# Kernel tuning notes

Measured on AMD Instinct MI355X. Metric: run time of the kernel, lower is better.

The kernel has to match this reference:

```python
import jax, jax.numpy as jnp
import numpy as np
from jax import lax

D_MODEL = 1024
D_STATE = 16
D_CONV = 4
EXPAND = 2
D_INNER = EXPAND * D_MODEL           # 2048 (mamba inner)
DT_RANK = (D_MODEL + 15) // 16       # 64
D_FF = 4 * D_MODEL                   # 4096 (SwiGLU hidden)
EPS = 1e-5
B, L = 2, 2048


def setup_inputs() -> dict:
    key = jax.random.key(0)
    ks = jax.random.split(key, 16)
    s = 0.02
    inp = {
        'x': jax.random.normal(ks[0], (B, L, D_MODEL), jnp.float32),
        'norm1_w': jnp.ones((D_MODEL,), jnp.float32),
        'norm2_w': jnp.ones((D_MODEL,), jnp.float32),
        # Mamba params (torch Linear convention: y = x @ W.T)
        'in_proj_w': s * jax.random.normal(ks[1], (2 * D_INNER, D_MODEL), jnp.float32),
        'conv_w': s * jax.random.normal(ks[2], (D_INNER, 1, D_CONV), jnp.float32),
        'conv_b': jnp.zeros((D_INNER,), jnp.float32),
        'x_proj_w': s * jax.random.normal(ks[3], (DT_RANK + 2 * D_STATE, D_INNER), jnp.float32),
        'dt_proj_w': s * jax.random.normal(ks[4], (D_INNER, DT_RANK), jnp.float32),
        'dt_proj_b': jax.random.uniform(ks[5], (D_INNER,), jnp.float32, -4.0, -2.0),
        'A_log': jnp.log(jnp.broadcast_to(jnp.arange(1, D_STATE + 1, dtype=jnp.float32), (D_INNER, D_STATE))),
        'D': jnp.ones((D_INNER,), jnp.float32),
        'out_proj_w': s * jax.random.normal(ks[6], (D_MODEL, D_INNER), jnp.float32),
        # SwiGLU MLP
        'w1': s * jax.random.normal(ks[7], (D_FF, D_MODEL), jnp.float32),
        'w2': s * jax.random.normal(ks[8], (D_FF, D_MODEL), jnp.float32),
        'w3': s * jax.random.normal(ks[9], (D_MODEL, D_FF), jnp.float32),
    }
    return inp


def _rmsnorm(x, w, eps=EPS):
    return x * lax.rsqrt(jnp.mean(x * x, axis=-1, keepdims=True) + eps) * w


def _mamba(x, in_proj_w, conv_w, conv_b, x_proj_w, dt_proj_w, dt_proj_b, A_log, Dp, out_proj_w):
    # x: (B, L, d_model)
    xz = x @ in_proj_w.T                       # (B, L, 2*d_inner)
    u, z = jnp.split(xz, 2, axis=-1)           # each (B, L, d_inner)
    # causal depthwise conv1d over time
    u_nch = u.transpose(0, 2, 1)               # (B, d_inner, L)
    u_conv = lax.conv_general_dilated(
        u_nch, conv_w, window_strides=(1,), padding=[(D_CONV - 1, 0)],
        dimension_numbers=('NCH', 'OIH', 'NCH'), feature_group_count=D_INNER)
    u_conv = u_conv + conv_b[None, :, None]
    u_act = jax.nn.silu(u_conv.transpose(0, 2, 1))   # (B, L, d_inner)
    # input-dependent dt, B, C
    proj = u_act @ x_proj_w.T                  # (B, L, dt_rank + 2*d_state)
    dt_r, Bm, Cm = jnp.split(proj, [DT_RANK, DT_RANK + D_STATE], axis=-1)
    dt = jax.nn.softplus(dt_r @ dt_proj_w.T + dt_proj_b)   # (B, L, d_inner)
    A = -jnp.exp(A_log)                        # (d_inner, d_state)
    dA = jnp.exp(jnp.einsum('bld,dn->bldn', dt, A))
    dBu = jnp.einsum('bld,bln,bld->bldn', dt, Bm, u_act)
    def step(h, inputs):
        dA_t, dBu_t = inputs                   # (B, d_inner, d_state)
        h = dA_t * h + dBu_t
        return h, h
    h0 = jnp.zeros((x.shape[0], D_INNER, D_STATE), x.dtype)
    _, hs = lax.scan(step, h0, (dA.transpose(1, 0, 2, 3), dBu.transpose(1, 0, 2, 3)))
    y = jnp.einsum('lbdn,bln->bld', hs, Cm) + u_act * Dp   # (B, L, d_inner)
    y = y * jax.nn.silu(z)
    return y @ out_proj_w.T                    # (B, L, d_model)


def reference(x, norm1_w, norm2_w, in_proj_w, conv_w, conv_b, x_proj_w,
              dt_proj_w, dt_proj_b, A_log, D, out_proj_w, w1, w2, w3):
    # residual + RMSNorm + Mamba (dropout = eval-mode identity)
    h = x + _mamba(_rmsnorm(x, norm1_w), in_proj_w, conv_w, conv_b,
                   x_proj_w, dt_proj_w, dt_proj_b, A_log, D, out_proj_w)
    # residual + RMSNorm + SwiGLU MLP
    xn = _rmsnorm(h, norm2_w)
    mlp = (jax.nn.silu(xn @ w1.T) * (xn @ w2.T)) @ w3.T
    return h + mlp
```

## Files before the change

### kernel.cpp

```cpp
#include <hip/hip_runtime.h>
#include <hip/hip_bf16.h>

#define TOKS 4096
#define DM   1024
#define DI   2048
#define DST  16
#define DTR  64
#define DFF  4096
#define PROJ_LD 128

#define NC    32
#define CHUNK 64

typedef __bf16 bf16x8 __attribute__((ext_vector_type(8)));
typedef float  f32x4  __attribute__((ext_vector_type(4)));

__device__ __forceinline__ __bf16 f2bf(float f) {
  union { float f; unsigned u; } v; v.f = f;
  unsigned r = v.u + 0x7fffu + ((v.u >> 16) & 1u);
  union { unsigned short s; __bf16 b; } o; o.s = (unsigned short)(r >> 16);
  return o.b;
}
__device__ __forceinline__ float siluf(float x) { return x / (1.f + __expf(-x)); }
__device__ __forceinline__ float softplusf(float x) { return x > 20.f ? x : log1pf(__expf(x)); }

__device__ __forceinline__ void gl2lds16(const void* g, void* l) {
  __builtin_amdgcn_global_load_lds((const __attribute__((address_space(1))) void*)g,
                                   (__attribute__((address_space(3))) void*)l, 16, 0, 0);
}

struct CvtArgs {
  const float* src[5];
  __bf16*      dst[5];
  int nblk[6];
};

__global__ __launch_bounds__(256) void cvt_bf16_kernel(CvtArgs a) {
  int blk = blockIdx.x;
  int seg = 0;
#pragma unroll
  for (int s = 1; s < 5; s++) if (blk >= a.nblk[s]) seg = s;
  size_t base = (size_t)(blk - a.nblk[seg]) * 2048 + threadIdx.x * 8;
  const float* src = a.src[seg] + base;
  __bf16*      dst = a.dst[seg] + base;
  float4 v0 = *(const float4*)src;
  float4 v1 = *(const float4*)(src + 4);
  union { __bf16 b[8]; uint4 u; } t;
  t.b[0]=f2bf(v0.x); t.b[1]=f2bf(v0.y); t.b[2]=f2bf(v0.z); t.b[3]=f2bf(v0.w);
  t.b[4]=f2bf(v1.x); t.b[5]=f2bf(v1.y); t.b[6]=f2bf(v1.z); t.b[7]=f2bf(v1.w);
  *(uint4*)dst = t.u;
}

__global__ __launch_bounds__(256) void cvt_w12_kernel(const float* __restrict__ w1,
                                                      const float* __restrict__ w2,
                                                      __bf16* __restrict__ dst) {
  int blk = blockIdx.x;
  int isw2 = blk >> 11;
  int b = blk & 2047;
  int r = b * 2 + (threadIdx.x >> 7);
  int col = (threadIdx.x & 127) * 8;
  const float* src = (isw2 ? w2 : w1) + (size_t)r * DM + col;
  int dr = (r >> 4) * 32 + (r & 15) + isw2 * 16;
  float4 v0 = *(const float4*)src;
  float4 v1 = *(const float4*)(src + 4);
  union { __bf16 b[8]; uint4 u; } t;
  t.b[0]=f2bf(v0.x); t.b[1]=f2bf(v0.y); t.b[2]=f2bf(v0.z); t.b[3]=f2bf(v0.w);
  t.b[4]=f2bf(v1.x); t.b[5]=f2bf(v1.y); t.b[6]=f2bf(v1.z); t.b[7]=f2bf(v1.w);
  *(uint4*)&dst[(size_t)dr * DM + col] = t.u;
}

__global__ __launch_bounds__(256) void rmsnorm_kernel(const float* __restrict__ x,
                                                      const float* __restrict__ w,
                                                      __bf16* __restrict__ out) {
  int row = blockIdx.x;
  const float* xr = x + (size_t)row * DM;
  float4 v = ((const float4*)xr)[threadIdx.x];
  float ss = v.x*v.x + v.y*v.y + v.z*v.z + v.w*v.w;
#pragma unroll
  for (int o = 32; o > 0; o >>= 1) ss += __shfl_xor(ss, o);
  __shared__ float sred[4];
  if ((threadIdx.x & 63) == 0) sred[threadIdx.x >> 6] = ss;
  __syncthreads();
  float tot = sred[0] + sred[1] + sred[2] + sred[3];
  float scale = rsqrtf(tot * (1.f / DM) + 1e-5f);
  float4 wv = ((const float4*)w)[threadIdx.x];
  union { __bf16 b[4]; ushort4 u; } o;
  o.b[0] = f2bf(v.x * scale * wv.x);
  o.b[1] = f2bf(v.y * scale * wv.y);
  o.b[2] = f2bf(v.z * scale * wv.z);
  o.b[3] = f2bf(v.w * scale * wv.w);
  *(ushort4*)&out[(size_t)row * DM + threadIdx.x * 4] = o.u;
}

template<int BM, int EPI, int SWAP, int KK, int Z, int LDA, int LDB, int LDC>
__global__ __launch_bounds__(256, BM == 128 ? 1 : 2) void gemm2(
    const void* __restrict__ Ap, const __bf16* __restrict__ Bp,
    void* __restrict__ Cp, const void* __restrict__ auxp)
{
  constexpr int FM = BM / 32;
  constexpr int AI = BM / 64;
  constexpr int kPer = KK / Z;
  __shared__ __bf16 sA[2][BM * 32];
  __shared__ __bf16 sB[2][128 * 32];
  const int tid  = threadIdx.x;
  const int wave = tid >> 6, lane = tid & 63;
  const int bm = SWAP ? blockIdx.x : blockIdx.y;
  const int bn = SWAP ? blockIdx.y : blockIdx.x;
  const int m0 = bm * BM, n0 = bn * 128;
  const int wr = wave >> 1, wc = wave & 1;
  const int frow = lane & 15, fq = lane >> 4;

  f32x4 acc[FM][4] = {};

  const int kBeg = (Z > 1) ? blockIdx.z * kPer : 0;
  const int kEnd = kBeg + kPer;

  const int lrow = lane >> 2;
  const int lcol = (lane & 3) * 8;

  auto stage = [&](int kt, int buf) {
#pragma unroll
    for (int q = 0; q < AI; q++) {
      int idx = wave * AI + q;
      gl2lds16((const __bf16*)Ap + (size_t)(m0 + idx * 16 + lrow) * LDA + kt + lcol,
               &sA[buf][idx * 512]);
    }
#pragma unroll
    for (int q = 0; q < 2; q++) {
      int idx = wave * 2 + q;
      gl2lds16(Bp + (size_t)(n0 + idx * 16 + lrow) * LDB + kt + lcol,
               &sB[buf][idx * 512]);
    }
  };

  stage(kBeg, 0);
  int cur = 0;
  for (int kt = kBeg; kt < kEnd; kt += 32) {
    __syncthreads();

    bf16x8 afr[FM], bfr[4];
#pragma unroll
    for (int i = 0; i < FM; i++)
      afr[i] = *(const bf16x8*)&sA[cur][(wr * (BM/2) + i * 16 + frow) * 32 + fq * 8];
#pragma unroll
    for (int j = 0; j < 4; j++)
      bfr[j] = *(const bf16x8*)&sB[cur][(wc * 64 + j * 16 + frow) * 32 + fq * 8];

    if (kt + 32 < kEnd) stage(kt + 32, cur ^ 1);

#pragma unroll
    for (int i = 0; i < FM; i++)
#pragma unroll
      for (int j = 0; j < 4; j++)
        acc[i][j] = __builtin_amdgcn_mfma_f32_16x16x32_bf16(afr[i], bfr[j], acc[i][j], 0, 0, 0);
    cur ^= 1;
  }

  const float* auxf = (const float*)auxp;
#pragma unroll
  for (int i = 0; i < FM; i++) {
    int gr = m0 + wr * (BM/2) + i * 16 + fq * 4;
#pragma unroll
    for (int j = 0; j < 4; j++) {
      int gc = n0 + wc * 64 + j * 16 + frow;
#pragma unroll
      for (int r = 0; r < 4; r++) {
        float v = acc[i][j][r];
        if (EPI == 6) {
          if (j & 1) {
            int col = (n0 >> 1) + 32 * wc + 16 * (j >> 1) + frow;
            size_t off = (size_t)(gr + r) * LDC + col;
            float g = acc[i][j-1][r];
            ((__bf16*)Cp)[off] = f2bf(siluf(g) * v);
          }
        } else {
          size_t off = (size_t)(gr + r) * LDC + gc;
          if (EPI == 1) ((__bf16*)Cp)[off] = f2bf(v);
          else if (EPI == 2) ((__bf16*)Cp)[off] = f2bf(softplusf(v + auxf[gc]));
          else if (EPI == 3) ((float*)Cp)[off] = v + auxf[off];
          else if (EPI == 7)
            ((float*)Cp)[(size_t)blockIdx.z * (TOKS * PROJ_LD) + off] = v;
        }
      }
    }
  }
}

template<int EPI, int KK, int LDA, int LDB, int LDC>
__global__ __launch_bounds__(512, 2) void gemm8(
    const __bf16* __restrict__ Ap, const __bf16* __restrict__ Bp,
    void* __restrict__ Cp)
{
  constexpr int NT = KK / 64;
  static_assert(NT % 2 == 0 && NT >= 4, "KK must be a multiple of 128");
  __shared__ alignas(16) char S[131072];

  const int tid  = threadIdx.x;
  const int wid  = tid >> 6, lane = tid & 63;
  const int wr   = wid >> 2, wc = wid & 3;
  const int m0   = blockIdx.y * 256, n0 = blockIdx.x * 256;
  const int frow = lane & 15, fq = lane >> 4;
  const int cbyt = (fq * 16) ^ (((lane >> 3) & 1) << 5);
  const int srow = lane >> 2;
  const int skin = ((lane & 3) * 8) ^ (((lane >> 5) & 1) << 4);

  const unsigned sbase = (unsigned)(size_t)(__attribute__((address_space(3))) char*)S;
  const unsigned abase = sbase + (unsigned)((wr * 64 + frow) * 64 + cbyt);
  const unsigned bbase = sbase + 32768u + (unsigned)((wc * 32 + frow) * 64 + cbyt);

  f32x4 acc[2][2][4][2] = {};
  bf16x8 fA[4][2], fB0[2][2], fB1[2][2];

#define G8_SB() __builtin_amdgcn_sched_barrier(0)
#define G8_BAR() do { G8_SB(); __builtin_amdgcn_s_barrier(); G8_SB(); } while (0)
#define G8_LGKM0() do { asm volatile("s_waitcnt lgkmcnt(0)"); G8_SB(); } while (0)
#define G8_THROT() asm volatile("s_waitcnt lgkmcnt(8)")
#define G8_WAIT6() asm volatile("s_waitcnt vmcnt(6)")
#define G8_WAIT0() asm volatile("s_waitcnt vmcnt(0)")
#define G8_DSR(dst, addr, OFF)                                                 \
    asm volatile("ds_read_b128 %0, %1 offset:" OFF : "=v"(dst) : "v"(addr))

#define G8_STAGE(buf, ab, h, tile) do {                                        \
    if ((tile) < NT) {                                                         \
      const __bf16* gb = (ab) ? Bp : Ap;                                       \
      const int ld = (ab) ? LDB : LDA;                                         \
      const int r0 = ((ab) ? n0 : m0) + (h) * 128;                             \
      _Pragma("unroll")                                                        \
      for (int q = 0; q < 2; q++) {                                            \
        int p = wid * 2 + q, kk = p >> 3, r16 = p & 7;                         \
        const __bf16* src = gb + (size_t)(r0 + r16 * 16 + srow) * ld           \
                            + (tile) * 64 + kk * 32 + skin;                    \
        char* dst = S + (((buf) * 4 + (ab) * 2 + kk) << 14)                    \
                    + ((h) * 128 + r16 * 16) * 64;                             \
        gl2lds16(src, dst);                                                    \
      }                                                                        \
    }                                                                          \
  } while (0)

#define G8_READ_A(buf, mh) do {                                                \
    unsigned a_ = abase + (buf) * 65536u + (mh) * 8192u;                       \
    f32x4 t0,t1,t2,t3,t4,t5,t6,t7;                                             \
    G8_DSR(t0, a_, "0");     G8_DSR(t1, a_, "1024");                           \
    G8_DSR(t2, a_, "2048");  G8_DSR(t3, a_, "3072");                           \
    G8_DSR(t4, a_, "16384"); G8_DSR(t5, a_, "17408");                          \
    G8_DSR(t6, a_, "18432"); G8_DSR(t7, a_, "19456");                          \
    fA[0][0]=__builtin_bit_cast(bf16x8,t0); fA[1][0]=__builtin_bit_cast(bf16x8,t1); \
    fA[2][0]=__builtin_bit_cast(bf16x8,t2); fA[3][0]=__builtin_bit_cast(bf16x8,t3); \
    fA[0][1]=__builtin_bit_cast(bf16x8,t4); fA[1][1]=__builtin_bit_cast(bf16x8,t5); \
    fA[2][1]=__builtin_bit_cast(bf16x8,t6); fA[3][1]=__builtin_bit_cast(bf16x8,t7); \
  } while (0)

#define G8_READ_B(buf, nh, FB) do {                                            \
    unsigned b_ = bbase + (buf) * 65536u + (nh) * 8192u;                       \
    f32x4 t0,t1,t2,t3;                                                         \
    G8_DSR(t0, b_, "0");     G8_DSR(t1, b_, "1024");                           \
    G8_DSR(t2, b_, "16384"); G8_DSR(t3, b_, "17408");                          \
    FB[0][0]=__builtin_bit_cast(bf16x8,t0); FB[1][0]=__builtin_bit_cast(bf16x8,t1); \
    FB[0][1]=__builtin_bit_cast(bf16x8,t2); FB[1][1]=__builtin_bit_cast(bf16x8,t3); \
  } while (0)

#define G8_MFMA(mh, nh, FB) do {                                               \
    __builtin_amdgcn_s_setprio(1);                                             \
    _Pragma("unroll")                                                          \
    for (int kk = 0; kk < 2; kk++)                                             \
      _Pragma("unroll")                                                        \
      for (int fi = 0; fi < 4; fi++)                                           \
        _Pragma("unroll")                                                      \
        for (int fj = 0; fj < 2; fj++)                                         \
          acc[mh][nh][fi][fj] = __builtin_amdgcn_mfma_f32_16x16x32_bf16(       \
              fA[fi][kk], FB[fj][kk], acc[mh][nh][fi][fj], 0, 0, 0);           \
    __builtin_amdgcn_s_setprio(0);                                             \
    G8_SB();                                                                   \
  } while (0)

  G8_STAGE(0, 0, 0, 0); G8_STAGE(0, 1, 1, 0); G8_STAGE(0, 0, 1, 0); G8_STAGE(0, 1, 0, 0);
  G8_STAGE(1, 0, 0, 1); G8_STAGE(1, 1, 1, 1); G8_STAGE(1, 0, 1, 1);
  G8_SB();
  G8_WAIT6();
  G8_BAR();

  for (int it = 0; it < NT / 2; ++it) {
    const int t1 = 2 * it + 1, t2 = 2 * it + 2, t3 = 2 * it + 3;
    const bool last = (it == NT / 2 - 1);
    G8_READ_A(0, 0); G8_READ_B(0, 0, fB0);
    G8_STAGE(1, 1, 0, t1);
    G8_SB(); G8_THROT();
    G8_BAR();
    G8_LGKM0();
    G8_MFMA(0, 0, fB0);
    G8_BAR();
    G8_READ_B(0, 1, fB1);
    G8_STAGE(0, 0, 0, t2);
    G8_SB();
    G8_BAR();
    G8_LGKM0();
    G8_MFMA(0, 1, fB1);
    G8_BAR();
    G8_READ_A(0, 1);
    G8_STAGE(0, 1, 1, t2);
    G8_SB();
    G8_BAR();
    G8_LGKM0();
    G8_MFMA(1, 1, fB1);
    G8_BAR();
    G8_STAGE(0, 0, 1, t2);
    G8_SB();
    if (last) G8_WAIT0(); else G8_WAIT6();
    G8_BAR();
    G8_MFMA(1, 0, fB0);
    G8_BAR();
    G8_READ_A(1, 0); G8_READ_B(1, 0, fB0);
    G8_STAGE(0, 1, 0, t2);
    G8_SB(); G8_THROT();
    G8_BAR();
    G8_LGKM0();
    G8_MFMA(0, 0, fB0);
    G8_BAR();
    G8_READ_B(1, 1, fB1);
    G8_STAGE(1, 0, 0, t3);
    G8_SB();
    G8_BAR();
    G8_LGKM0();
    G8_MFMA(0, 1, fB1);
    G8_BAR();
    G8_READ_A(1, 1);
    G8_STAGE(1, 1, 1, t3);
    G8_SB();
    G8_BAR();
    G8_LGKM0();
    G8_MFMA(1, 1, fB1);
    G8_BAR();
    G8_STAGE(1, 0, 1, t3);
    G8_SB();
    if (!last) G8_WAIT6();
    G8_BAR();
    G8_MFMA(1, 0, fB0);
    G8_BAR();
  }

#undef G8_STAGE
#undef G8_READ_A
#undef G8_READ_B
#undef G8_MFMA
#undef G8_BAR
#undef G8_SB
#undef G8_LGKM0
#undef G8_THROT
#undef G8_WAIT6
#undef G8_WAIT0
#undef G8_DSR

#pragma unroll
  for (int mh = 0; mh < 2; mh++)
#pragma unroll
    for (int nh = 0; nh < 2; nh++)
#pragma unroll
      for (int fi = 0; fi < 4; fi++) {
        int gr = m0 + mh * 128 + wr * 64 + fi * 16 + fq * 4;
        if constexpr (EPI == 1) {
#pragma unroll
          for (int fj = 0; fj < 2; fj++) {
            int gc = n0 + nh * 128 + wc * 32 + fj * 16 + frow;
#pragma unroll
            for (int r = 0; r < 4; r++)
              ((__bf16*)Cp)[(size_t)(gr + r) * LDC + gc] = f2bf(acc[mh][nh][fi][fj][r]);
          }
        } else {
          int col = ((n0 + nh * 128 + wc * 32) >> 1) + frow;
#pragma unroll
          for (int r = 0; r < 4; r++) {
            float g = acc[mh][nh][fi][0][r];
            float v = acc[mh][nh][fi][1][r];
            ((__bf16*)Cp)[(size_t)(gr + r) * LDC + col] = f2bf(siluf(g) * v);
          }
        }
      }
}

__global__ __launch_bounds__(256) void xp_reduce_kernel(const float* __restrict__ part,
                                                        float* __restrict__ proj,
                                                        __bf16* __restrict__ projb) {
  int i = blockIdx.x * 256 + threadIdx.x;
  float4 s = ((const float4*)part)[i];
#pragma unroll
  for (int z = 1; z < 8; z++) {
    float4 v = ((const float4*)(part + (size_t)z * TOKS * PROJ_LD))[i];
    s.x += v.x; s.y += v.y; s.z += v.z; s.w += v.w;
  }
  ((float4*)proj)[i] = s;
  int c4 = i & 31;
  if (c4 < 16) {
    int tok = i >> 5;
    union { __bf16 b[4]; ushort4 u; } t;
    t.b[0]=f2bf(s.x); t.b[1]=f2bf(s.y); t.b[2]=f2bf(s.z); t.b[3]=f2bf(s.w);
    *(ushort4*)&projb[(size_t)tok * 64 + c4 * 4] = t.u;
  }
}

__global__ __launch_bounds__(256) void conv_silu_kernel(const __bf16* __restrict__ xz,
                                                        const float* __restrict__ cw,
                                                        const float* __restrict__ cb,
                                                        __bf16* __restrict__ uact) {
  int idx = blockIdx.x * 256 + threadIdx.x;
  int d   = idx & (DI - 1);
  int tok = idx >> 11;
  int l   = tok & 2047;
  float4 wv = *(const float4*)(cw + d * 4);
  const __bf16* up = xz + (size_t)tok * (2 * DI) + d;
  float acc = cb[d];
  if (l >= 3) acc += wv.x * (float)up[-3 * (2 * DI)];
  if (l >= 2) acc += wv.y * (float)up[-2 * (2 * DI)];
  if (l >= 1) acc += wv.z * (float)up[-1 * (2 * DI)];
  acc += wv.w * (float)up[0];
  uact[idx] = f2bf(siluf(acc));
}

__global__ __launch_bounds__(64) void scan_pass1(const __bf16* __restrict__ dt,
                                                 const __bf16* __restrict__ uact,
                                                 const float* __restrict__ proj,
                                                 const float* __restrict__ A_log,
                                                 float* __restrict__ aprod,
                                                 float* __restrict__ hend) {
  int lane = threadIdx.x;
  int d = blockIdx.x * 64 + lane;
  int c = blockIdx.y, b = blockIdx.z;
  float An[16], h[16], ap[16];
  {
    const float4* a4 = (const float4*)(A_log + (size_t)d * 16);
#pragma unroll
    for (int q = 0; q < 4; q++) {
      float4 v = a4[q];
      An[q*4+0] = -__expf(v.x); An[q*4+1] = -__expf(v.y);
      An[q*4+2] = -__expf(v.z); An[q*4+3] = -__expf(v.w);
    }
  }
#pragma unroll
  for (int n = 0; n < 16; n++) { h[n] = 0.f; ap[n] = 1.f; }

  size_t tok = (size_t)b * 2048 + (size_t)c * CHUNK;
  const __bf16* dtp = dt   + tok * DI + d;
  const __bf16* up  = uact + tok * DI + d;
  const float*  pp  = proj + tok * PROJ_LD;

  for (int t = 0; t < CHUNK; t++) {
    float dtv = (float)*dtp;
    float uv  = (float)*up;
    const float4* b4 = (const float4*)(pp + 64);
    float Bv[16];
#pragma unroll
    for (int q = 0; q < 4; q++) {
      float4 v = b4[q];
      Bv[q*4+0]=v.x; Bv[q*4+1]=v.y; Bv[q*4+2]=v.z; Bv[q*4+3]=v.w;
    }
    float du = dtv * uv;
#pragma unroll
    for (int n = 0; n < 16; n++) {
      float dA = __expf(dtv * An[n]);
      ap[n] *= dA;
      h[n] = fmaf(dA, h[n], du * Bv[n]);
    }
    dtp += DI; up += DI; pp += PROJ_LD;
  }

  size_t off = ((size_t)(b * NC + c) * DI + d) * 16;
#pragma unroll
  for (int q = 0; q < 4; q++) {
    *(float4*)(hend  + off + q*4) = make_float4(h[q*4+0],  h[q*4+1],  h[q*4+2],  h[q*4+3]);
    *(float4*)(aprod + off + q*4) = make_float4(ap[q*4+0], ap[q*4+1], ap[q*4+2], ap[q*4+3]);
  }
}

__global__ __launch_bounds__(256) void scan_pass2(const float* __restrict__ aprod,
                                                  const float* __restrict__ hend,
                                                  float* __restrict__ hstart) {
  int idx = blockIdx.x * 256 + threadIdx.x;
  int b  = idx >> 13;
  int r4 = idx & 8191;
  float4 H = make_float4(0.f, 0.f, 0.f, 0.f);
  for (int c = 0; c < NC; c++) {
    size_t off = (size_t)(b * NC + c) * (DI * 16 / 4) + r4;
    ((float4*)hstart)[off] = H;
    float4 a = ((const float4*)aprod)[off];
    float4 e = ((const float4*)hend)[off];
    H.x = fmaf(a.x, H.x, e.x);
    H.y = fmaf(a.y, H.y, e.y);
    H.z = fmaf(a.z, H.z, e.z);
    H.w = fmaf(a.w, H.w, e.w);
  }
}

__global__ __launch_bounds__(64) void scan_pass3(const __bf16* __restrict__ dt,
                                                 const __bf16* __restrict__ uact,
                                                 const float* __restrict__ proj,
                                                 const __bf16* __restrict__ xz,
                                                 const float* __restrict__ A_log,
                                                 const float* __restrict__ Dp,
                                                 const float* __restrict__ hstart,
                                                 __bf16* __restrict__ y) {
  int lane = threadIdx.x;
  int d = blockIdx.x * 64 + lane;
  int c = blockIdx.y, b = blockIdx.z;
  float An[16], h[16];
  {
    const float4* a4 = (const float4*)(A_log + (size_t)d * 16);
#pragma unroll
    for (int q = 0; q < 4; q++) {
      float4 v = a4[q];
      An[q*4+0] = -__expf(v.x); An[q*4+1] = -__expf(v.y);
      An[q*4+2] = -__expf(v.z); An[q*4+3] = -__expf(v.w);
    }
  }
  {
    size_t off = ((size_t)(b * NC + c) * DI + d) * 16;
#pragma unroll
    for (int q = 0; q < 4; q++) {
      float4 v = *(const float4*)(hstart + off + q*4);
      h[q*4+0]=v.x; h[q*4+1]=v.y; h[q*4+2]=v.z; h[q*4+3]=v.w;
    }
  }
  float Dd = Dp[d];

  size_t tok = (size_t)b * 2048 + (size_t)c * CHUNK;
  const __bf16* dtp = dt   + tok * DI + d;
  const __bf16* up  = uact + tok * DI + d;
  const float*  pp  = proj + tok * PROJ_LD;
  const __bf16* zp  = xz   + tok * (2 * DI) + DI + d;
  __bf16*       yp  = y    + tok * DI + d;

  for (int t = 0; t < CHUNK; t++) {
    float dtv = (float)*dtp;
    float uv  = (float)*up;
    float zv  = (float)*zp;
    const float4* b4 = (const float4*)(pp + 64);
    float Bv[16], Cv[16];
#pragma unroll
    for (int q = 0; q < 4; q++) {
      float4 v = b4[q];
      Bv[q*4+0]=v.x; Bv[q*4+1]=v.y; Bv[q*4+2]=v.z; Bv[q*4+3]=v.w;
      float4 w = b4[q + 4];
      Cv[q*4+0]=w.x; Cv[q*4+1]=w.y; Cv[q*4+2]=w.z; Cv[q*4+3]=w.w;
    }
    float du = dtv * uv;
    float p = 0.f;
#pragma unroll
    for (int n = 0; n < 16; n++) {
      float dA = __expf(dtv * An[n]);
      h[n] = fmaf(dA, h[n], du * Bv[n]);
      p = fmaf(h[n], Cv[n], p);
    }
    *yp = f2bf((p + Dd * uv) * siluf(zv));
    dtp += DI; up += DI; pp += PROJ_LD; zp += 2 * DI; yp += DI;
  }
}

extern "C" void kernel_launch(void* const* d_in, const int* in_sizes, int n_in,
                              void* d_out, int out_size, void* d_ws, size_t ws_size,
                              hipStream_t stream) {
  const float* x        = (const float*)d_in[0];
  const float* n1w      = (const float*)d_in[1];
  const float* n2w      = (const float*)d_in[2];
  const float* in_projw = (const float*)d_in[3];
  const float* conv_w   = (const float*)d_in[4];
  const float* conv_b   = (const float*)d_in[5];
  const float* x_projw  = (const float*)d_in[6];
  const float* dt_projw = (const float*)d_in[7];
  const float* dt_projb = (const float*)d_in[8];
  const float* A_log    = (const float*)d_in[9];
  const float* Dp       = (const float*)d_in[10];
  const float* out_projw= (const float*)d_in[11];
  const float* w1       = (const float*)d_in[12];
  const float* w2       = (const float*)d_in[13];
  const float* w3       = (const float*)d_in[14];
  float* out = (float*)d_out;

  char* ws = (char*)d_ws;
  __bf16* xz   = (__bf16*)(ws + 0);
  __bf16* uact = (__bf16*)(ws + 33554432);
  float*  proj = (float*) (ws + 50331648);
  __bf16* dt   = (__bf16*)(ws + 52428800);
  __bf16* yb   = (__bf16*)(ws + 85983232);
  float*  xpp  = (float*) (ws + 85983232);
  float*  h    = (float*) (ws + 102760448);
  __bf16* xn   = (__bf16*)(ws + 119537664);
  __bf16* hid  = xz;
  __bf16* projb = (__bf16*)(ws + 102760448);
  float* aprod  = (float*)(ws + 102760448);
  float* hend   = (float*)(ws + 111149056);
  float* hstart = (float*)(ws + 119537664);
  char* wb = ws + 127926272;
  __bf16* b_in  = (__bf16*)(wb);
  __bf16* b_xp  = (__bf16*)(wb + 8388608);
  __bf16* b_dtp = (__bf16*)(wb + 8912896);
  __bf16* b_out = (__bf16*)(wb + 9175040);
  __bf16* b_w12 = (__bf16*)(wb + 13369344);
  __bf16* b_w3  = (__bf16*)(wb + 30146560);

  hipMemsetAsync(b_xp, 0, 128 * 2048 * sizeof(__bf16), stream);

  CvtArgs ca;
  const float* srcs[5] = {in_projw, x_projw, dt_projw, out_projw, w3};
  __bf16* dsts[5]      = {b_in, b_xp, b_dtp, b_out, b_w3};
  int counts[5] = {4096*1024, 96*2048, 2048*64, 1024*2048, 1024*4096};
  int acc = 0;
  for (int i = 0; i < 5; i++) { ca.src[i] = srcs[i]; ca.dst[i] = dsts[i]; ca.nblk[i] = acc; acc += counts[i] / 2048; }
  ca.nblk[5] = acc;
  cvt_bf16_kernel<<<acc, 256, 0, stream>>>(ca);
  cvt_w12_kernel<<<4096, 256, 0, stream>>>(w1, w2, b_w12);

  dim3 blk(256);
  rmsnorm_kernel<<<TOKS, 256, 0, stream>>>(x, n1w, xn);
  gemm8<1, 1024, DM, DM, 4096><<<dim3(16, 16), 512, 0, stream>>>(xn, b_in, xz);
  conv_silu_kernel<<<(TOKS*DI)/256, 256, 0, stream>>>(xz, conv_w, conv_b, uact);
  gemm2<64,7,0, 2048,8, DI,DI,PROJ_LD><<<dim3(1,64,8), blk, 0, stream>>>(uact, b_xp, xpp, nullptr);
  xp_reduce_kernel<<<512, 256, 0, stream>>>(xpp, proj, projb);
  gemm2<128,2,0, 64,1, 64,DTR,DI><<<dim3(16,32,1), blk, 0, stream>>>(projb, b_dtp, dt, dt_projb);
  scan_pass1<<<dim3(DI/64, NC, 2), 64, 0, stream>>>(dt, uact, proj, A_log, aprod, hend);
  scan_pass2<<<64, 256, 0, stream>>>(aprod, hend, hstart);
  scan_pass3<<<dim3(DI/64, NC, 2), 64, 0, stream>>>(dt, uact, proj, xz, A_log, Dp, hstart, yb);
  gemm2<64,3,1, 2048,1, DI,DI,DM><<<dim3(64,8,1), blk, 0, stream>>>(yb, b_out, h, x);
  rmsnorm_kernel<<<TOKS, 256, 0, stream>>>(h, n2w, xn);
  gemm8<6, 1024, DM, DM, DFF><<<dim3(32, 16), 512, 0, stream>>>(xn, b_w12, hid);
  gemm2<64,3,1, 4096,1, DFF,DFF,DM><<<dim3(64,8,1), blk, 0, stream>>>(hid, b_w3, out, h);

  (void)in_sizes; (void)n_in; (void)out_size; (void)ws_size;
}
```

Baseline: 522.5 us.

## Split-K the output GEMMs, fuse reduction with residual and RMSNorm, vectorize conv

Measured after the change: 536.7 us. +2.7%, slower.

```diff
diff --git a/kernel.cpp b/kernel.cpp
--- a/kernel.cpp
+++ b/kernel.cpp
@@ -92,8 +92,49 @@
   *(ushort4*)&out[(size_t)row * DM + threadIdx.x * 4] = o.u;
 }
 
+__global__ __launch_bounds__(256) void rmsnorm_red3_kernel(const float* __restrict__ p,
+                                                           const float* __restrict__ xres,
+                                                           const float* __restrict__ w,
+                                                           float* __restrict__ hout,
+                                                           __bf16* __restrict__ out) {
+  int row = blockIdx.x;
+  size_t base = (size_t)row * DM + threadIdx.x * 4;
+  float4 a = *(const float4*)(p + base);
+  float4 b = *(const float4*)(p + (size_t)TOKS * DM + base);
+  float4 c = *(const float4*)(xres + base);
+  float4 v = make_float4(a.x + b.x + c.x, a.y + b.y + c.y,
+                         a.z + b.z + c.z, a.w + b.w + c.w);
+  *(float4*)(hout + base) = v;
+  float ss = v.x*v.x + v.y*v.y + v.z*v.z + v.w*v.w;
+#pragma unroll
+  for (int o = 32; o > 0; o >>= 1) ss += __shfl_xor(ss, o);
+  __shared__ float sred[4];
+  if ((threadIdx.x & 63) == 0) sred[threadIdx.x >> 6] = ss;
+  __syncthreads();
+  float tot = sred[0] + sred[1] + sred[2] + sred[3];
+  float scale = rsqrtf(tot * (1.f / DM) + 1e-5f);
+  float4 wv = ((const float4*)w)[threadIdx.x];
+  union { __bf16 b[4]; ushort4 u; } o;
+  o.b[0] = f2bf(v.x * scale * wv.x);
+  o.b[1] = f2bf(v.y * scale * wv.y);
+  o.b[2] = f2bf(v.z * scale * wv.z);
+  o.b[3] = f2bf(v.w * scale * wv.w);
+  *(ushort4*)&out[base] = o.u;
+}
+
+__global__ __launch_bounds__(256) void add_red2_kernel(const float* __restrict__ p,
+                                                       const float* __restrict__ aux,
+                                                       float* __restrict__ out) {
+  int i = blockIdx.x * 256 + threadIdx.x;
+  float4 a = ((const float4*)p)[i];
+  float4 b = ((const float4*)(p + (size_t)TOKS * DM))[i];
+  float4 c = ((const float4*)aux)[i];
+  ((float4*)out)[i] = make_float4(a.x + b.x + c.x, a.y + b.y + c.y,
+                                  a.z + b.z + c.z, a.w + b.w + c.w);
+}
+
 template<int BM, int EPI, int SWAP, int KK, int Z, int LDA, int LDB, int LDC>
-__global__ __launch_bounds__(256, BM == 128 ? 1 : 2) void gemm2(
+__global__ __launch_bounds__(256, BM == 128 ? 1 : 4) void gemm2(
     const void* __restrict__ Ap, const __bf16* __restrict__ Bp,
     void* __restrict__ Cp, const void* __restrict__ auxp)
 {
@@ -180,6 +221,8 @@
           else if (EPI == 3) ((float*)Cp)[off] = v + auxf[off];
           else if (EPI == 7)
             ((float*)Cp)[(size_t)blockIdx.z * (TOKS * PROJ_LD) + off] = v;
+          else if (EPI == 8)
+            ((float*)Cp)[(size_t)blockIdx.z * ((size_t)TOKS * LDC) + off] = v;
         }
       }
     }
@@ -402,17 +445,30 @@
                                                         const float* __restrict__ cb,
                                                         __bf16* __restrict__ uact) {
   int idx = blockIdx.x * 256 + threadIdx.x;
-  int d   = idx & (DI - 1);
-  int tok = idx >> 11;
+  int d8  = (idx & 255) * 8;
+  int tok = idx >> 8;
   int l   = tok & 2047;
-  float4 wv = *(const float4*)(cw + d * 4);
-  const __bf16* up = xz + (size_t)tok * (2 * DI) + d;
-  float acc = cb[d];
-  if (l >= 3) acc += wv.x * (float)up[-3 * (2 * DI)];
-  if (l >= 2) acc += wv.y * (float)up[-2 * (2 * DI)];
-  if (l >= 1) acc += wv.z * (float)up[-1 * (2 * DI)];
-  acc += wv.w * (float)up[0];
-  uact[idx] = f2bf(siluf(acc));
+  const __bf16* up = xz + (size_t)tok * (2 * DI) + d8;
+  bf16x8 u0 = {}, u1 = {}, u2 = {}, u3;
+  if (l >= 3) u0 = *(const bf16x8*)(up - 3 * (2 * DI));
+  if (l >= 2) u1 = *(const bf16x8*)(up - 2 * (2 * DI));
+  if (l >= 1) u2 = *(const bf16x8*)(up - 1 * (2 * DI));
+  u3 = *(const bf16x8*)up;
+  float4 cb0 = *(const float4*)(cb + d8);
+  float4 cb1 = *(const float4*)(cb + d8 + 4);
+  float cbv[8] = {cb0.x, cb0.y, cb0.z, cb0.w, cb1.x, cb1.y, cb1.z, cb1.w};
+  union { __bf16 b[8]; uint4 u; } res;
+#pragma unroll
+  for (int j = 0; j < 8; j++) {
+    float4 wv = *(const float4*)(cw + (size_t)(d8 + j) * 4);
+    float acc = cbv[j];
+    acc += wv.x * (float)u0[j];
+    acc += wv.y * (float)u1[j];
+    acc += wv.z * (float)u2[j];
+    acc += wv.w * (float)u3[j];
+    res.b[j] = f2bf(siluf(acc));
+  }
+  *(uint4*)&uact[(size_t)tok * DI + d8] = res.u;
 }
 
 __global__ __launch_bounds__(64) void scan_pass1(const __bf16* __restrict__ dt,
@@ -587,6 +643,7 @@
   float* aprod  = (float*)(ws + 102760448);
   float* hend   = (float*)(ws + 111149056);
   float* hstart = (float*)(ws + 119537664);
+  float* pk = (float*)(ws + 52428800);
   char* wb = ws + 127926272;
   __bf16* b_in  = (__bf16*)(wb);
   __bf16* b_xp  = (__bf16*)(wb + 8388608);
@@ -610,17 +667,18 @@
   dim3 blk(256);
   rmsnorm_kernel<<<TOKS, 256, 0, stream>>>(x, n1w, xn);
   gemm8<1, 1024, DM, DM, 4096><<<dim3(16, 16), 512, 0, stream>>>(xn, b_in, xz);
-  conv_silu_kernel<<<(TOKS*DI)/256, 256, 0, stream>>>(xz, conv_w, conv_b, uact);
+  conv_silu_kernel<<<(TOKS*DI/8)/256, 256, 0, stream>>>(xz, conv_w, conv_b, uact);
   gemm2<64,7,0, 2048,8, DI,DI,PROJ_LD><<<dim3(1,64,8), blk, 0, stream>>>(uact, b_xp, xpp, nullptr);
   xp_reduce_kernel<<<512, 256, 0, stream>>>(xpp, proj, projb);
   gemm2<128,2,0, 64,1, 64,DTR,DI><<<dim3(16,32,1), blk, 0, stream>>>(projb, b_dtp, dt, dt_projb);
   scan_pass1<<<dim3(DI/64, NC, 2), 64, 0, stream>>>(dt, uact, proj, A_log, aprod, hend);
   scan_pass2<<<64, 256, 0, stream>>>(aprod, hend, hstart);
   scan_pass3<<<dim3(DI/64, NC, 2), 64, 0, stream>>>(dt, uact, proj, xz, A_log, Dp, hstart, yb);
-  gemm2<64,3,1, 2048,1, DI,DI,DM><<<dim3(64,8,1), blk, 0, stream>>>(yb, b_out, h, x);
-  rmsnorm_kernel<<<TOKS, 256, 0, stream>>>(h, n2w, xn);
+  gemm2<64,8,1, 2048,2, DI,DI,DM><<<dim3(64,8,2), blk, 0, stream>>>(yb, b_out, pk, nullptr);
+  rmsnorm_red3_kernel<<<TOKS, 256, 0, stream>>>(pk, x, n2w, h, xn);
   gemm8<6, 1024, DM, DM, DFF><<<dim3(32, 16), 512, 0, stream>>>(xn, b_w12, hid);
-  gemm2<64,3,1, 4096,1, DFF,DFF,DM><<<dim3(64,8,1), blk, 0, stream>>>(hid, b_w3, out, h);
+  gemm2<64,8,1, 4096,2, DFF,DFF,DM><<<dim3(64,8,2), blk, 0, stream>>>(hid, b_w3, pk, nullptr);
+  add_red2_kernel<<<(TOKS*DM/4)/256, 256, 0, stream>>>(pk, h, out);
 
   (void)in_sizes; (void)n_in; (void)out_size; (void)ws_size;
 }
```
